# Kernel optimization log

Hardware: AMD Instinct MI355X
Metric: run time of the kernel (lower is better)

## Reference

```python
import jax, jax.numpy as jnp
import numpy as np

B, S, H_IN, H = 32, 1024, 1024, 1024


def setup_inputs() -> dict:
    key = jax.random.key(0)
    k1, k2, k3, k4, k5, k6, k7 = jax.random.split(key, 7)
    hidden = jax.random.normal(k1, (B, H), dtype=jnp.float32)
    encoder_outputs = jax.random.normal(k2, (S, B, H_IN), dtype=jnp.float32)
    mask = jax.random.randint(k3, (B, S), 0, 2).astype(bool)
    mask = mask.at[:, 0].set(False)  # ensure at least one unmasked position per row
    lim1 = 1.0 / np.sqrt(H_IN + H)
    lim2 = 1.0 / np.sqrt(H)
    W1 = jax.random.uniform(k4, (H, H_IN + H), minval=-lim1, maxval=lim1, dtype=jnp.float32)
    b1 = jax.random.uniform(k5, (H,), minval=-lim1, maxval=lim1, dtype=jnp.float32)
    W2 = jax.random.uniform(k6, (1, H), minval=-lim2, maxval=lim2, dtype=jnp.float32)
    b2 = jax.random.uniform(k7, (1,), minval=-lim2, maxval=lim2, dtype=jnp.float32)
    return {"hidden": hidden, "encoder_outputs": encoder_outputs, "mask": mask,
            "W1": W1, "b1": b1, "W2": W2, "b2": b2}


def reference(hidden, encoder_outputs, mask, W1, b1, W2, b2):
    # encoder_outputs: [S,B,Hin] -> [B,S,Hin]; hidden: [B,H] broadcast over S.
    enc = jnp.transpose(encoder_outputs, (1, 0, 2))  # [B,S,Hin]
    # cat([enc, hidden], -1) @ W1.T == enc @ W1_enc.T + hidden @ W1_hid.T (avoids materializing concat)
    W1_enc, W1_hid = W1[:, :enc.shape[-1]], W1[:, enc.shape[-1]:]
    a1 = jnp.einsum('bsi,hi->bsh', enc, W1_enc) + (hidden @ W1_hid.T)[:, None, :] + b1
    a1 = jnp.tanh(a1)                                # [B,S,H]
    scores = jnp.einsum('bsh,h->bs', a1, W2[0]) + b2[0]  # [B,S]
    scores = jnp.where(mask, -jnp.inf, scores)
    attn = jax.nn.softmax(scores, axis=-1)           # softmax over seq dim
    return attn[:, None, :]                          # [B,1,S]
```

## Files before the change

### kernel.cpp

```cpp
#include <hip/hip_runtime.h>
#include <hip/hip_bf16.h>
#include <cstdint>


#define BK 64
#define NKT 16

typedef short  s16x8 __attribute__((ext_vector_type(8)));
typedef float  f32x4 __attribute__((ext_vector_type(4)));
typedef unsigned int u32;
typedef unsigned short u16;
typedef unsigned long long u64;

__device__ static inline u32 f2bf(float f) {
    u32 u = __float_as_uint(f);
    return (u + 0x7fffu + ((u >> 16) & 1u)) >> 16;
}
__device__ static inline u32 pk2(float a, float b) {
    return f2bf(a) | (f2bf(b) << 16);
}

__device__ static inline void gload_lds16(const void* g, void* l) {
    __builtin_amdgcn_global_load_lds(
        (const __attribute__((address_space(1))) u32*)g,
        (__attribute__((address_space(3))) u32*)l, 16, 0, 0);
}

__global__ __launch_bounds__(256) void prep_k(const float* __restrict__ W1,
                                              const float* __restrict__ hidden,
                                              const float* __restrict__ b1,
                                              const void*  __restrict__ maskv,
                                              u16*   __restrict__ Wb,
                                              float* __restrict__ hv,
                                              int*   __restrict__ sidx,
                                              int*   __restrict__ cnt,
                                              float* __restrict__ scores) {
    const int bx = blockIdx.x, t = threadIdx.x;
    const int wid = t >> 6, lane = t & 63;
    __shared__ int sflag[4];

    if (bx < 512) {
        const int i = bx * 256 + t;
        const int n = i >> 7, gc = i & 127;
        const float4 v0 = *(const float4*)(W1 + (size_t)n * 2048 + gc * 8);
        const float4 v1 = *(const float4*)(W1 + (size_t)n * 2048 + gc * 8 + 4);
        uint4 o; o.x = pk2(v0.x, v0.y); o.y = pk2(v0.z, v0.w);
        o.z = pk2(v1.x, v1.y); o.w = pk2(v1.z, v1.w);
        *(uint4*)(Wb + (size_t)n * 1024 + gc * 8) = o;
    } else if (bx < 768) {
        const int h = (bx - 512) * 4 + wid;
        const float4* wrow = (const float4*)(W1 + (size_t)h * 2048 + 1024);
        float4 w[4];
#pragma unroll
        for (int q = 0; q < 4; q++) w[q] = wrow[lane + 64 * q];
        for (int b = 0; b < 32; b++) {
            const float4* hb = (const float4*)(hidden + (size_t)b * 1024);
            float p = 0.f;
#pragma unroll
            for (int q = 0; q < 4; q++) {
                float4 x = hb[lane + 64 * q];
                p = fmaf(w[q].x, x.x, fmaf(w[q].y, x.y, fmaf(w[q].z, x.z, fmaf(w[q].w, x.w, p))));
            }
#pragma unroll
            for (int off = 1; off < 64; off <<= 1) p += __shfl_xor(p, off);
            if (lane == 0) hv[(size_t)b * 1024 + h] = p + b1[h];
        }
    } else if (bx < 776) {
        const u32* mw = (const u32*)maskv;
        int f = 0;
#pragma unroll
        for (int j = 0; j < 32; j++) f |= (mw[t * 32 + j] > 1u) ? 1 : 0;
        const int anyf = __any(f);
        if (lane == 0) sflag[wid] = anyf;
        __syncthreads();
        const int bytemode = sflag[0] | sflag[1] | sflag[2] | sflag[3];

        const int b = (bx - 768) * 4 + wid;
        int base = 0;
        for (int c = 0; c < 16; c++) {
            const int s = c * 64 + lane;
            int m;
            if (bytemode) m = ((const unsigned char*)maskv)[(size_t)b * 1024 + s];
            else          m = ((const int*)maskv)[(size_t)b * 1024 + s];
            const u64 bal = __ballot(m == 0);
            if (m == 0) {
                const int off = (int)__popcll(bal & ((1ull << lane) - 1ull));
                sidx[(size_t)b * 1024 + base + off] = s;
            }
            base += (int)__popcll(bal);
        }
        if (lane == 0) cnt[b] = base;
        for (int j = base + lane; j < 1024; j += 64) sidx[(size_t)b * 1024 + j] = 0;
    } else {
        const int i = (bx - 776) * 256 + t;
        ((float4*)scores)[i] = make_float4(0.f, 0.f, 0.f, 0.f);
    }
}

__global__ __launch_bounds__(256) void conv_k(const float* __restrict__ enc,
                                              const int* __restrict__ sidx,
                                              const int* __restrict__ cnt,
                                              u16* __restrict__ encC) {
    const int bid = blockIdx.x, t = threadIdx.x;
    const int xcd = bid & 7, w = bid >> 3;
    const int b = xcd * 4 + (w >> 8);
    const int j0 = (w & 255) * 4;
    const int c = cnt[b];
    if (j0 >= ((c + 127) & ~127)) return;
#pragma unroll
    for (int r = 0; r < 4; r++) {
        const int j = j0 + r;
        const int s = (j < c) ? sidx[(size_t)b * 1024 + j] : 0;
        const float4 v = ((const float4*)(enc + ((size_t)s * 32 + b) * 1024))[t];
        uint2 o; o.x = pk2(v.x, v.y); o.y = pk2(v.z, v.w);
        *(uint2*)(encC + ((size_t)b * 1024 + j) * 1024 + t * 4) = o;
    }
}

__global__ __launch_bounds__(256, 6) void gemm_s(
    const u16* __restrict__ encC,
    const u16* __restrict__ Wb,
    const int* __restrict__ sidx,
    const int* __restrict__ cnt,
    const float* __restrict__ hv,
    const float* __restrict__ W2,
    float*      __restrict__ scores)
{
    __shared__ u16 As[64 * BK];
    __shared__ u16 Bs[128 * BK];

    const int tid = threadIdx.x;
    const int bid = blockIdx.x;
    const int xcd = bid & 7, idx = bid >> 3;
    const int strip = xcd * 64 + (idx >> 3);
    const int nt = idx & 7;
    const int b = strip >> 4, mt = strip & 15;
    const int c = cnt[b];
    if (mt * 64 >= c) return;

    const int srow = tid >> 3, sc16 = tid & 7;
    const u16* asrc = encC + ((size_t)b * 1024 + mt * 64 + srow) * 1024 + sc16 * 8;
    const u16* bsrc = Wb + ((size_t)(nt * 128) + srow) * 1024 + sc16 * 8;

    const int wid = tid >> 6, lane = tid & 63;
    const int wr = wid >> 1, wc = wid & 1;
    const int lhi = lane >> 4, llo = lane & 15;

    f32x4 acc[2][4] = {};

    for (int kt = 0; kt < NKT; kt++) {
        const size_t ko = (size_t)kt * 64;
#pragma unroll
        for (int j = 0; j < 2; j++)
            gload_lds16(asrc + ko + (size_t)j * 32 * 1024, &As[(j * 256 + tid) * 8]);
#pragma unroll
        for (int j = 0; j < 4; j++)
            gload_lds16(bsrc + ko + (size_t)j * 32 * 1024, &Bs[(j * 256 + tid) * 8]);
        __syncthreads();
#pragma unroll
        for (int kk = 0; kk < 2; kk++) {
            s16x8 af[2], bfr[4];
#pragma unroll
            for (int f = 0; f < 2; f++)
                af[f] = *(const s16x8*)&As[(wr * 32 + f * 16 + llo) * BK + kk * 32 + lhi * 8];
#pragma unroll
            for (int f = 0; f < 4; f++)
                bfr[f] = *(const s16x8*)&Bs[(wc * 64 + f * 16 + llo) * BK + kk * 32 + lhi * 8];
#pragma unroll
            for (int fi = 0; fi < 2; fi++)
#pragma unroll
                for (int fj = 0; fj < 4; fj++)
                    acc[fi][fj] = __builtin_amdgcn_mfma_f32_16x16x32_bf16(af[fi], bfr[fj], acc[fi][fj], 0, 0, 0);
        }
        __syncthreads();
    }

    const float* hvb = hv + (size_t)b * 1024;
    float hvv[4], w2v[4];
#pragma unroll
    for (int fj = 0; fj < 4; fj++) {
        const int n = nt * 128 + wc * 64 + fj * 16 + llo;
        hvv[fj] = hvb[n];
        w2v[fj] = W2[n];
    }
#pragma unroll
    for (int fi = 0; fi < 2; fi++) {
#pragma unroll
        for (int r = 0; r < 4; r++) {
            float sum = 0.f;
#pragma unroll
            for (int fj = 0; fj < 4; fj++) {
                const float x = acc[fi][fj][r] + hvv[fj];
                const float e = __expf(2.f * x);
                const float t = 1.f - 2.f / (e + 1.f);
                sum = fmaf(t, w2v[fj], sum);
            }
            sum += __shfl_xor(sum, 1);
            sum += __shfl_xor(sum, 2);
            sum += __shfl_xor(sum, 4);
            sum += __shfl_xor(sum, 8);
            if (llo == 0) {
                const int j = mt * 64 + wr * 32 + fi * 16 + lhi * 4 + r;
                if (j < c) {
                    const int s = sidx[(size_t)b * 1024 + j];
                    atomicAdd(&scores[(size_t)b * 1024 + s], sum);
                }
            }
        }
    }
}

__global__ __launch_bounds__(256) void softmax_k(const float* __restrict__ scores,
                                                 const void* __restrict__ maskv,
                                                 float* __restrict__ out) {
    const int b = blockIdx.x, t = threadIdx.x;
    const int wid = t >> 6, lane = t & 63;
    const u32* mw = (const u32*)maskv;
    int f = 0;
#pragma unroll
    for (int j = 0; j < 32; j++) f |= (mw[t * 32 + j] > 1u) ? 1 : 0;
    __shared__ int sflag[4];
    const int anyf = __any(f);
    if (lane == 0) sflag[wid] = anyf;
    __syncthreads();
    const int bytemode = sflag[0] | sflag[1] | sflag[2] | sflag[3];

    int m0, m1, m2, m3;
    if (bytemode) {
        const uchar4 mk = ((const uchar4*)((const unsigned char*)maskv + (size_t)b * 1024))[t];
        m0 = mk.x; m1 = mk.y; m2 = mk.z; m3 = mk.w;
    } else {
        const int4 mk = ((const int4*)((const int*)maskv + (size_t)b * 1024))[t];
        m0 = mk.x; m1 = mk.y; m2 = mk.z; m3 = mk.w;
    }
    const float4 sc = ((const float4*)(scores + (size_t)b * 1024))[t];
    const float v0 = m0 ? -1e30f : sc.x;
    const float v1 = m1 ? -1e30f : sc.y;
    const float v2 = m2 ? -1e30f : sc.z;
    const float v3 = m3 ? -1e30f : sc.w;
    float mx = fmaxf(fmaxf(v0, v1), fmaxf(v2, v3));
#pragma unroll
    for (int off = 1; off < 64; off <<= 1) mx = fmaxf(mx, __shfl_xor(mx, off));
    __shared__ float redm[4], reds[4];
    if (lane == 0) redm[wid] = mx;
    __syncthreads();
    mx = fmaxf(fmaxf(redm[0], redm[1]), fmaxf(redm[2], redm[3]));
    const float e0 = m0 ? 0.f : __expf(v0 - mx);
    const float e1 = m1 ? 0.f : __expf(v1 - mx);
    const float e2 = m2 ? 0.f : __expf(v2 - mx);
    const float e3 = m3 ? 0.f : __expf(v3 - mx);
    float s = e0 + e1 + e2 + e3;
#pragma unroll
    for (int off = 1; off < 64; off <<= 1) s += __shfl_xor(s, off);
    if (lane == 0) reds[wid] = s;
    __syncthreads();
    s = reds[0] + reds[1] + reds[2] + reds[3];
    const float inv = 1.f / s;
    float4 o; o.x = e0 * inv; o.y = e1 * inv; o.z = e2 * inv; o.w = e3 * inv;
    ((float4*)(out + (size_t)b * 1024))[t] = o;
}

extern "C" void kernel_launch(void* const* d_in, const int* in_sizes, int n_in,
                              void* d_out, int out_size, void* d_ws, size_t ws_size,
                              hipStream_t stream) {
    const float* hidden = (const float*)d_in[0];
    const float* enc    = (const float*)d_in[1];
    const void*  mask   = d_in[2];
    const float* W1 = (const float*)d_in[3];
    const float* b1 = (const float*)d_in[4];
    const float* W2 = (const float*)d_in[5];
    float* out = (float*)d_out;

    char* ws = (char*)d_ws;
    float* ws_scores = (float*)ws;
    float* ws_hv     = (float*)(ws + (128u << 10));
    u16*   ws_Wb     = (u16*)(ws + (256u << 10));
    int*   ws_cnt    = (int*)(ws + (2304u << 10));
    int*   ws_sidx   = (int*)(ws + (2432u << 10));
    u16*   ws_encC   = (u16*)(ws + (4096u << 10));

    prep_k<<<808, 256, 0, stream>>>(W1, hidden, b1, mask, ws_Wb, ws_hv, ws_sidx, ws_cnt, ws_scores);
    conv_k<<<8192, 256, 0, stream>>>(enc, ws_sidx, ws_cnt, ws_encC);
    gemm_s<<<4096, 256, 0, stream>>>(ws_encC, ws_Wb, ws_sidx, ws_cnt, ws_hv, W2, ws_scores);
    softmax_k<<<32, 256, 0, stream>>>(ws_scores, mask, out);
}
```

Measured before the change: 116.7 us.

## Pre-swizzle operands into MFMA fragment layout and drop LDS staging in GEMM

The prep and conversion kernels now write W1 and the compacted encoder rows in a fragment-major layout matching the MFMA 16x16x32 lane order. The GEMM can then load each lane's fragment straight from global memory with no LDS tiles and no barriers. The aim is to remove LDS traffic and synchronisation stalls. The cost is that operands shared across waves are re-read from global/L2 with no software double-buffering, and occupancy bounds change from 6 to 4.

```diff
diff --git a/kernel.cpp b/kernel.cpp
--- a/kernel.cpp
+++ b/kernel.cpp
@@ -2,9 +2,6 @@
 #include <hip/hip_bf16.h>
 #include <cstdint>
 
-
-#define BK 64
-#define NKT 16
 
 typedef short  s16x8 __attribute__((ext_vector_type(8)));
 typedef float  f32x4 __attribute__((ext_vector_type(4)));
@@ -20,17 +17,11 @@
     return f2bf(a) | (f2bf(b) << 16);
 }
 
-__device__ static inline void gload_lds16(const void* g, void* l) {
-    __builtin_amdgcn_global_load_lds(
-        (const __attribute__((address_space(1))) u32*)g,
-        (__attribute__((address_space(3))) u32*)l, 16, 0, 0);
-}
-
 __global__ __launch_bounds__(256) void prep_k(const float* __restrict__ W1,
                                               const float* __restrict__ hidden,
                                               const float* __restrict__ b1,
                                               const void*  __restrict__ maskv,
-                                              u16*   __restrict__ Wb,
+                                              u16*   __restrict__ Wfrag,
                                               float* __restrict__ hv,
                                               int*   __restrict__ sidx,
                                               int*   __restrict__ cnt,
@@ -41,12 +32,15 @@
 
     if (bx < 512) {
         const int i = bx * 256 + t;
-        const int n = i >> 7, gc = i & 127;
-        const float4 v0 = *(const float4*)(W1 + (size_t)n * 2048 + gc * 8);
-        const float4 v1 = *(const float4*)(W1 + (size_t)n * 2048 + gc * 8 + 4);
+        const int llo = i & 15, lhi = (i >> 4) & 3;
+        const int kk = (i >> 6) & 1, kt = (i >> 7) & 15, rt = i >> 11;
+        const int n = rt * 16 + llo;
+        const int kb = kt * 64 + kk * 32 + lhi * 8;
+        const float4 v0 = *(const float4*)(W1 + (size_t)n * 2048 + kb);
+        const float4 v1 = *(const float4*)(W1 + (size_t)n * 2048 + kb + 4);
         uint4 o; o.x = pk2(v0.x, v0.y); o.y = pk2(v0.z, v0.w);
         o.z = pk2(v1.x, v1.y); o.w = pk2(v1.z, v1.w);
-        *(uint4*)(Wb + (size_t)n * 1024 + gc * 8) = o;
+        *(uint4*)(Wfrag + (size_t)i * 8) = o;
     } else if (bx < 768) {
         const int h = (bx - 512) * 4 + wid;
         const float4* wrow = (const float4*)(W1 + (size_t)h * 2048 + 1024);
@@ -100,7 +94,7 @@
 __global__ __launch_bounds__(256) void conv_k(const float* __restrict__ enc,
                                               const int* __restrict__ sidx,
                                               const int* __restrict__ cnt,
-                                              u16* __restrict__ encC) {
+                                              u16* __restrict__ encF) {
     const int bid = blockIdx.x, t = threadIdx.x;
     const int xcd = bid & 7, w = bid >> 3;
     const int b = xcd * 4 + (w >> 8);
@@ -108,27 +102,32 @@
     const int c = cnt[b];
     if (j0 >= ((c + 127) & ~127)) return;
 #pragma unroll
-    for (int r = 0; r < 4; r++) {
-        const int j = j0 + r;
+    for (int p = 0; p < 2; p++) {
+        const int q = t + p * 256;
+        const int jl = q >> 7, c8 = q & 127;
+        const int j = j0 + jl;
         const int s = (j < c) ? sidx[(size_t)b * 1024 + j] : 0;
-        const float4 v = ((const float4*)(enc + ((size_t)s * 32 + b) * 1024))[t];
-        uint2 o; o.x = pk2(v.x, v.y); o.y = pk2(v.z, v.w);
-        *(uint2*)(encC + ((size_t)b * 1024 + j) * 1024 + t * 4) = o;
-    }
-}
-
-__global__ __launch_bounds__(256, 6) void gemm_s(
-    const u16* __restrict__ encC,
-    const u16* __restrict__ Wb,
+        const float* src = enc + ((size_t)s * 32 + b) * 1024 + c8 * 8;
+        const float4 v0 = *(const float4*)src;
+        const float4 v1 = *(const float4*)(src + 4);
+        const int rt = j >> 4, llo = j & 15;
+        const int kt = c8 >> 3, kk = (c8 >> 2) & 1, lhi = c8 & 3;
+        const size_t a16 = (((size_t)b * 64 + rt) * 32 + kt * 2 + kk) * 64 + lhi * 16 + llo;
+        uint4 o; o.x = pk2(v0.x, v0.y); o.y = pk2(v0.z, v0.w);
+        o.z = pk2(v1.x, v1.y); o.w = pk2(v1.z, v1.w);
+        *(uint4*)(encF + a16 * 8) = o;
+    }
+}
+
+__global__ __launch_bounds__(256, 4) void gemm_flat(
+    const u16* __restrict__ encF,
+    const u16* __restrict__ Wfrag,
     const int* __restrict__ sidx,
     const int* __restrict__ cnt,
     const float* __restrict__ hv,
     const float* __restrict__ W2,
     float*      __restrict__ scores)
 {
-    __shared__ u16 As[64 * BK];
-    __shared__ u16 Bs[128 * BK];
-
     const int tid = threadIdx.x;
     const int bid = blockIdx.x;
     const int xcd = bid & 7, idx = bid >> 3;
@@ -138,41 +137,34 @@
     const int c = cnt[b];
     if (mt * 64 >= c) return;
 
-    const int srow = tid >> 3, sc16 = tid & 7;
-    const u16* asrc = encC + ((size_t)b * 1024 + mt * 64 + srow) * 1024 + sc16 * 8;
-    const u16* bsrc = Wb + ((size_t)(nt * 128) + srow) * 1024 + sc16 * 8;
-
     const int wid = tid >> 6, lane = tid & 63;
     const int wr = wid >> 1, wc = wid & 1;
     const int lhi = lane >> 4, llo = lane & 15;
 
+    const u16* Abase = encF + (((size_t)b * 64 + mt * 4 + wr * 2) * 32 * 64 + lane) * 8;
+    const u16* Bbase = Wfrag + (((size_t)nt * 8 + wc * 4) * 32 * 64 + lane) * 8;
+
     f32x4 acc[2][4] = {};
 
-    for (int kt = 0; kt < NKT; kt++) {
-        const size_t ko = (size_t)kt * 64;
-#pragma unroll
-        for (int j = 0; j < 2; j++)
-            gload_lds16(asrc + ko + (size_t)j * 32 * 1024, &As[(j * 256 + tid) * 8]);
-#pragma unroll
-        for (int j = 0; j < 4; j++)
-            gload_lds16(bsrc + ko + (size_t)j * 32 * 1024, &Bs[(j * 256 + tid) * 8]);
-        __syncthreads();
+#pragma unroll 2
+    for (int kt = 0; kt < 16; kt++) {
 #pragma unroll
         for (int kk = 0; kk < 2; kk++) {
-            s16x8 af[2], bfr[4];
-#pragma unroll
-            for (int f = 0; f < 2; f++)
-                af[f] = *(const s16x8*)&As[(wr * 32 + f * 16 + llo) * BK + kk * 32 + lhi * 8];
-#pragma unroll
-            for (int f = 0; f < 4; f++)
-                bfr[f] = *(const s16x8*)&Bs[(wc * 64 + f * 16 + llo) * BK + kk * 32 + lhi * 8];
+            const int off = (kt * 2 + kk) * 512;
+            s16x8 af[2], bf[4];
 #pragma unroll
             for (int fi = 0; fi < 2; fi++)
+                af[fi] = *(const s16x8*)(Abase + off + fi * 16384);
+#pragma unroll
+            for (int fj = 0; fj < 4; fj++)
+                bf[fj] = *(const s16x8*)(Bbase + off + fj * 16384);
+#pragma unroll
+            for (int fi = 0; fi < 2; fi++)
 #pragma unroll
                 for (int fj = 0; fj < 4; fj++)
-                    acc[fi][fj] = __builtin_amdgcn_mfma_f32_16x16x32_bf16(af[fi], bfr[fj], acc[fi][fj], 0, 0, 0);
-        }
-        __syncthreads();
+                    acc[fi][fj] = __builtin_amdgcn_mfma_f32_16x16x32_bf16(
+                        af[fi], bf[fj], acc[fi][fj], 0, 0, 0);
+        }
     }
 
     const float* hvb = hv + (size_t)b * 1024;
@@ -277,10 +269,10 @@
     u16*   ws_Wb     = (u16*)(ws + (256u << 10));
     int*   ws_cnt    = (int*)(ws + (2304u << 10));
     int*   ws_sidx   = (int*)(ws + (2432u << 10));
-    u16*   ws_encC   = (u16*)(ws + (4096u << 10));
+    u16*   ws_encF   = (u16*)(ws + (4096u << 10));
 
     prep_k<<<808, 256, 0, stream>>>(W1, hidden, b1, mask, ws_Wb, ws_hv, ws_sidx, ws_cnt, ws_scores);
-    conv_k<<<8192, 256, 0, stream>>>(enc, ws_sidx, ws_cnt, ws_encC);
-    gemm_s<<<4096, 256, 0, stream>>>(ws_encC, ws_Wb, ws_sidx, ws_cnt, ws_hv, W2, ws_scores);
+    conv_k<<<8192, 256, 0, stream>>>(enc, ws_sidx, ws_cnt, ws_encF);
+    gemm_flat<<<4096, 256, 0, stream>>>(ws_encF, ws_Wb, ws_sidx, ws_cnt, ws_hv, W2, ws_scores);
     softmax_k<<<32, 256, 0, stream>>>(ws_scores, mask, out);
 }
```

After: 123.8 us. 6.1% more time.
